# Kernel optimization log

Measured on AMD Instinct MI355X. Metric: run time of the kernel, lower is better.

The kernel has to match this reference:

```python
import jax, jax.numpy as jnp
import numpy as np

N, M1, M2, D, S0, S1 = 60000, 40000, 40000, 64, 10, 20

def setup_inputs() -> dict:
    key = jax.random.key(0)
    ks = jax.random.split(key, 10)
    return {
        "h0": jax.random.normal(ks[0], (N, D), jnp.float32),
        "h1": jax.random.normal(ks[1], (M1, D), jnp.float32),
        "h2": jax.random.normal(ks[2], (M2, D), jnp.float32),
        "nei0": jax.random.randint(ks[3], (N, S0), 0, M1),
        "nei1": jax.random.randint(ks[4], (N, S1), 0, M2),
        "att_w0": jax.random.normal(ks[5], (1, 2 * D), jnp.float32) * 0.15,
        "att_w1": jax.random.normal(ks[6], (1, 2 * D), jnp.float32) * 0.15,
        "fc_w": jax.random.normal(ks[7], (D, D), jnp.float32) * 0.15,
        "fc_b": jnp.zeros((D,), jnp.float32),
        "fus_att_w": jax.random.normal(ks[8], (1, D), jnp.float32) * 0.15,
        "glob_att": jax.random.normal(ks[9], (1, D), jnp.float32) * 0.15,
        "gate": jnp.float32(0.8),
    }

def _nei_att(nei, h, h_refer, att_w):
    # F.embedding gather: [N, S, D]
    nei_emb = h[nei]
    d = h.shape[-1]
    # concat([h_refer, nei_emb]) @ att.T == h_refer@a_ref + nei_emb@a_nei
    a_ref, a_nei = att_w[0, :d], att_w[0, d:]
    scores = (h_refer @ a_ref)[:, None] + nei_emb @ a_nei  # [N, S]
    scores = jax.nn.leaky_relu(scores, 0.01)
    w = jax.nn.softmax(scores, axis=1)  # softmax over neighbors
    return jnp.einsum('ns,nsd->nd', w, nei_emb)

def reference(h0, h1, h2, nei0, nei1, att_w0, att_w1, fc_w, fc_b, fus_att_w, glob_att, gate):
    # intra (per neighbor type) attention + elu
    e0 = jax.nn.elu(_nei_att(nei0, h1, h0, att_w0))
    e1 = jax.nn.elu(_nei_att(nei1, h2, h0, att_w1))
    # fus_att (inter-type semantic attention)
    def beta_of(e):
        sp = jnp.tanh(e @ fc_w.T + fc_b)
        return (sp @ fus_att_w[0]).mean()
    beta = jax.nn.softmax(jnp.stack([beta_of(e0), beta_of(e1)]))
    z_mc = beta[0] * e0 + beta[1] * e1
    # global encoder: softmax over all nodes of all types
    all_nodes = jnp.concatenate([h0, h1, h2], axis=0)
    s = (all_nodes @ glob_att[0]) / jnp.sqrt(jnp.float32(D))
    w = jax.nn.softmax(s, axis=0)[:, None]
    global_embed = (w * all_nodes).sum(axis=0)  # [D]
    # weighted gate fusion
    gv = jax.nn.sigmoid(gate)
    return gv * z_mc + (1.0 - gv) * global_embed
```

## Files before the change

### kernel.cpp

```cpp
#include <hip/hip_runtime.h>
#include <math.h>

#define N_NODES 60000
#define M1_N    40000
#define M2_N    40000
#define DD      64
#define S0_N    10
#define S1_N    20
#define R_TOTAL (N_NODES + M1_N + M2_N)
#define T_H0    (N_NODES / 16)
#define T_H1    (T_H0 + M1_N / 16)
#define T_ALL   (T_H1 + M2_N / 16)
#define PROJ_GRID 2048
#define BETA_GRID 512

typedef __attribute__((ext_vector_type(8))) short short8;
typedef __attribute__((ext_vector_type(4))) float f32x4;

__device__ __forceinline__ float wave_sum(float x) {
#pragma unroll
    for (int o = 32; o >= 1; o >>= 1) x += __shfl_xor(x, o, 64);
    return x;
}
__device__ __forceinline__ float bcast(float v, int l) {
    return __uint_as_float(__builtin_amdgcn_readlane(__float_as_uint(v), l));
}
__device__ __forceinline__ float tanh_fast(float x) {
    return 1.f - 2.f / (__expf(2.f * x) + 1.f);
}
__device__ __forceinline__ unsigned short f2bf(float x) {
    unsigned u = __float_as_uint(x);
    return (unsigned short)((u + 0x7FFFu + ((u >> 16) & 1u)) >> 16);
}
__device__ __forceinline__ float bf2f(unsigned short u) {
    return __uint_as_float(((unsigned)u) << 16);
}

__global__ __launch_bounds__(256) void k_proj(
    const float* __restrict__ h0, const float* __restrict__ h1, const float* __restrict__ h2,
    const float* __restrict__ aw0, const float* __restrict__ aw1, const float* __restrict__ gatt,
    float* __restrict__ part,
    float* __restrict__ p0r0, float* __restrict__ p0r1,
    float* __restrict__ p1, float* __restrict__ p2,
    unsigned short* __restrict__ h1bf, unsigned short* __restrict__ h2bf)
{
    __shared__ float s_wsum[64];
    __shared__ float s_se;
    const int tid = threadIdx.x, lane = tid & 63, wid = tid >> 6;
    if (tid < 64) s_wsum[tid] = 0.f;
    if (tid == 0) s_se = 0.f;
    __syncthreads();

    const int m = lane & 15, quad = lane >> 4;

    short8 b0, b1;
    {
        const float* vsel = 0;
        if (m == 1) vsel = aw0;
        else if (m == 2) vsel = aw1;
        else if (m == 3) vsel = aw0 + DD;
        else if (m == 4) vsel = aw1 + DD;
        else if (m == 0) vsel = gatt;
#pragma unroll
        for (int j = 0; j < 8; j++) {
            b0[j] = vsel ? (short)f2bf(vsel[quad * 8 + j]) : (short)0;
            b1[j] = vsel ? (short)f2bf(vsel[32 + quad * 8 + j]) : (short)0;
        }
    }

    float wacc0[8], wacc1[8];
#pragma unroll
    for (int j = 0; j < 8; j++) { wacc0[j] = 0.f; wacc1[j] = 0.f; }
    float r_se = 0.f;

    const int srcl = (m >> 2) << 4;
    const int rsel = m & 3;

    const int gw = blockIdx.x * 4 + wid, nw = gridDim.x * 4;
    for (int tile = gw; tile < T_ALL; tile += nw) {
        const float* src; int rbase, region;
        if (tile < T_H0)      { src = h0; rbase = tile * 16;          region = 0; }
        else if (tile < T_H1) { src = h1; rbase = (tile - T_H0) * 16; region = 1; }
        else                  { src = h2; rbase = (tile - T_H1) * 16; region = 2; }
        const int row = rbase + m;
        const float4* rpa = (const float4*)(src + (size_t)row * DD + quad * 8);
        const float4* rpb = (const float4*)(src + (size_t)row * DD + 32 + quad * 8);
        const float4 va = rpa[0], vb = rpa[1];
        const float4 vc = rpb[0], vd = rpb[1];

        short8 a0, a1;
        a0[0] = (short)f2bf(va.x); a0[1] = (short)f2bf(va.y);
        a0[2] = (short)f2bf(va.z); a0[3] = (short)f2bf(va.w);
        a0[4] = (short)f2bf(vb.x); a0[5] = (short)f2bf(vb.y);
        a0[6] = (short)f2bf(vb.z); a0[7] = (short)f2bf(vb.w);
        a1[0] = (short)f2bf(vc.x); a1[1] = (short)f2bf(vc.y);
        a1[2] = (short)f2bf(vc.z); a1[3] = (short)f2bf(vc.w);
        a1[4] = (short)f2bf(vd.x); a1[5] = (short)f2bf(vd.y);
        a1[6] = (short)f2bf(vd.z); a1[7] = (short)f2bf(vd.w);

        f32x4 c = {0.f, 0.f, 0.f, 0.f};
        c = __builtin_amdgcn_mfma_f32_16x16x32_bf16(a0, b0, c, 0, 0, 0);
        c = __builtin_amdgcn_mfma_f32_16x16x32_bf16(a1, b1, c, 0, 0, 0);

        const float t0 = __shfl(c[0], srcl, 64);
        const float t1 = __shfl(c[1], srcl, 64);
        const float t2 = __shfl(c[2], srcl, 64);
        const float t3 = __shfl(c[3], srcl, 64);
        const float scr = (rsel == 0) ? t0 : (rsel == 1) ? t1 : (rsel == 2) ? t2 : t3;
        const float es = __expf(scr * 0.125f);
        r_se += es;
        wacc0[0] = fmaf(es, va.x, wacc0[0]); wacc0[1] = fmaf(es, va.y, wacc0[1]);
        wacc0[2] = fmaf(es, va.z, wacc0[2]); wacc0[3] = fmaf(es, va.w, wacc0[3]);
        wacc0[4] = fmaf(es, vb.x, wacc0[4]); wacc0[5] = fmaf(es, vb.y, wacc0[5]);
        wacc0[6] = fmaf(es, vb.z, wacc0[6]); wacc0[7] = fmaf(es, vb.w, wacc0[7]);
        wacc1[0] = fmaf(es, vc.x, wacc1[0]); wacc1[1] = fmaf(es, vc.y, wacc1[1]);
        wacc1[2] = fmaf(es, vc.z, wacc1[2]); wacc1[3] = fmaf(es, vc.w, wacc1[3]);
        wacc1[4] = fmaf(es, vd.x, wacc1[4]); wacc1[5] = fmaf(es, vd.y, wacc1[5]);
        wacc1[6] = fmaf(es, vd.z, wacc1[6]); wacc1[7] = fmaf(es, vd.w, wacc1[7]);

        if (region == 0) {
            if (m == 1) { float4 t = {c[0], c[1], c[2], c[3]}; *(float4*)(p0r0 + rbase + quad * 4) = t; }
            if (m == 2) { float4 t = {c[0], c[1], c[2], c[3]}; *(float4*)(p0r1 + rbase + quad * 4) = t; }
        } else if (region == 1) {
            if (m == 3) { float4 t = {c[0], c[1], c[2], c[3]}; *(float4*)(p1 + rbase + quad * 4) = t; }
            *(short8*)(h1bf + (size_t)row * DD + quad * 8) = a0;
            *(short8*)(h1bf + (size_t)row * DD + 32 + quad * 8) = a1;
        } else {
            if (m == 4) { float4 t = {c[0], c[1], c[2], c[3]}; *(float4*)(p2 + rbase + quad * 4) = t; }
            *(short8*)(h2bf + (size_t)row * DD + quad * 8) = a0;
            *(short8*)(h2bf + (size_t)row * DD + 32 + quad * 8) = a1;
        }
    }

    r_se *= 0.25f;
#pragma unroll
    for (int o = 1; o <= 8; o <<= 1) {
#pragma unroll
        for (int j = 0; j < 8; j++) {
            wacc0[j] += __shfl_xor(wacc0[j], o, 64);
            wacc1[j] += __shfl_xor(wacc1[j], o, 64);
        }
    }
    if (m == 0) {
#pragma unroll
        for (int j = 0; j < 8; j++) {
            atomicAdd(&s_wsum[quad * 8 + j],      wacc0[j]);
            atomicAdd(&s_wsum[32 + quad * 8 + j], wacc1[j]);
        }
    }
    const float se = wave_sum(r_se);
    if (lane == 0) atomicAdd(&s_se, se);
    __syncthreads();
    if (tid < 64) part[tid * PROJ_GRID + blockIdx.x] = s_wsum[tid];
    if (tid == 64) part[64 * PROJ_GRID + blockIdx.x] = s_se;
}

__global__ __launch_bounds__(256) void k_attn(
    const unsigned short* __restrict__ h1bf,
    const int* __restrict__ nei0, const int* __restrict__ nei1,
    const float* __restrict__ p0r0, const float* __restrict__ p0r1,
    const float* __restrict__ p1,
    unsigned short* __restrict__ e0bf, unsigned short* __restrict__ e1bf)
{
    const int tid = threadIdx.x, lane = tid & 63, wid = tid >> 6;
    const int sub = lane & 15, grp = lane >> 4;
    const int gw = blockIdx.x * 4 + wid;
    const int nw = gridDim.x * 4;

    for (int n = gw; n < N_NODES; n += nw) {
        int idx = 0; float w = 0.f;
        if (lane < S0_N) {
            idx = nei0[n * S0_N + lane];
            float sc = p0r0[n] + p1[idx];
            sc = (sc >= 0.f) ? sc : 0.01f * sc;
            w = __expf(sc);
        }
        int r0[3];
#pragma unroll
        for (int j = 0; j < 3; j++) r0[j] = __shfl(idx, 4 * j + grp, 64);
        ushort4 u0[3];
#pragma unroll
        for (int j = 0; j < 3; j++)
            u0[j] = *(const ushort4*)(h1bf + r0[j] * DD + 4 * sub);

        float sv = w;
#pragma unroll
        for (int o = 8; o >= 1; o >>= 1) sv += __shfl_xor(sv, o, 64);
        const float inv = 1.f / bcast(sv, 0);

        float w0[3];
#pragma unroll
        for (int j = 0; j < 3; j++) w0[j] = __shfl(w, 4 * j + grp, 64);

        float4 a = make_float4(0.f, 0.f, 0.f, 0.f);
#pragma unroll
        for (int j = 0; j < 3; j++) {
            a.x = fmaf(w0[j], bf2f(u0[j].x), a.x);
            a.y = fmaf(w0[j], bf2f(u0[j].y), a.y);
            a.z = fmaf(w0[j], bf2f(u0[j].z), a.z);
            a.w = fmaf(w0[j], bf2f(u0[j].w), a.w);
        }
#pragma unroll
        for (int o = 16; o <= 32; o <<= 1) {
            a.x += __shfl_xor(a.x, o, 64); a.y += __shfl_xor(a.y, o, 64);
            a.z += __shfl_xor(a.z, o, 64); a.w += __shfl_xor(a.w, o, 64);
        }
        if (grp == 0) {
            float4 e;
            e.x = a.x * inv; e.y = a.y * inv; e.z = a.z * inv; e.w = a.w * inv;
            e.x = (e.x > 0.f) ? e.x : (__expf(e.x) - 1.f);
            e.y = (e.y > 0.f) ? e.y : (__expf(e.y) - 1.f);
            e.z = (e.z > 0.f) ? e.z : (__expf(e.z) - 1.f);
            e.w = (e.w > 0.f) ? e.w : (__expf(e.w) - 1.f);
            ushort4 s; s.x = f2bf(e.x); s.y = f2bf(e.y); s.z = f2bf(e.z); s.w = f2bf(e.w);
            *(ushort4*)(e0bf + n * DD + 4 * sub) = s;
        }
    }

    for (int n = gw; n < N_NODES; n += nw) {
        int idx = 0; float w = 0.f;
        if (lane < S1_N) {
            idx = nei1[n * S1_N + lane] + M1_N;
            float sc = p0r1[n] + p1[idx];
            sc = (sc >= 0.f) ? sc : 0.01f * sc;
            w = __expf(sc);
        }
        int r1[5];
#pragma unroll
        for (int j = 0; j < 5; j++) r1[j] = __shfl(idx, 4 * j + grp, 64);
        ushort4 u1[5];
#pragma unroll
        for (int j = 0; j < 5; j++)
            u1[j] = *(const ushort4*)(h1bf + r1[j] * DD + 4 * sub);

        float sv = w;
#pragma unroll
        for (int o = 16; o >= 1; o >>= 1) sv += __shfl_xor(sv, o, 64);
        const float inv = 1.f / bcast(sv, 0);

        float w1[5];
#pragma unroll
        for (int j = 0; j < 5; j++) w1[j] = __shfl(w, 4 * j + grp, 64);

        float4 a = make_float4(0.f, 0.f, 0.f, 0.f);
#pragma unroll
        for (int j = 0; j < 5; j++) {
            a.x = fmaf(w1[j], bf2f(u1[j].x), a.x);
            a.y = fmaf(w1[j], bf2f(u1[j].y), a.y);
            a.z = fmaf(w1[j], bf2f(u1[j].z), a.z);
            a.w = fmaf(w1[j], bf2f(u1[j].w), a.w);
        }
#pragma unroll
        for (int o = 16; o <= 32; o <<= 1) {
            a.x += __shfl_xor(a.x, o, 64); a.y += __shfl_xor(a.y, o, 64);
            a.z += __shfl_xor(a.z, o, 64); a.w += __shfl_xor(a.w, o, 64);
        }
        if (grp == 0) {
            float4 e;
            e.x = a.x * inv; e.y = a.y * inv; e.z = a.z * inv; e.w = a.w * inv;
            e.x = (e.x > 0.f) ? e.x : (__expf(e.x) - 1.f);
            e.y = (e.y > 0.f) ? e.y : (__expf(e.y) - 1.f);
            e.z = (e.z > 0.f) ? e.z : (__expf(e.z) - 1.f);
            e.w = (e.w > 0.f) ? e.w : (__expf(e.w) - 1.f);
            ushort4 s; s.x = f2bf(e.x); s.y = f2bf(e.y); s.z = f2bf(e.z); s.w = f2bf(e.w);
            *(ushort4*)(e1bf + n * DD + 4 * sub) = s;
        }
    }
}

__global__ __launch_bounds__(256) void k_beta(
    const unsigned short* __restrict__ e0bf, const unsigned short* __restrict__ e1bf,
    const float* __restrict__ fcw, const float* __restrict__ fcb,
    const float* __restrict__ fus, float* __restrict__ bpart)
{
    __shared__ float s_part[2];
    const int tid = threadIdx.x, lane = tid & 63, wid = tid >> 6;
    if (tid < 2) s_part[tid] = 0.f;
    const int m = lane & 15, q = lane >> 4;

    short8 bfr[4][2];
    float fb[4], fu[4];
#pragma unroll
    for (int t = 0; t < 4; t++) {
        const float* wrow = fcw + (t * 16 + m) * DD;
#pragma unroll
        for (int h = 0; h < 2; h++) {
            const float* p = wrow + h * 32 + q * 8;
#pragma unroll
            for (int j = 0; j < 8; j++) bfr[t][h][j] = (short)f2bf(p[j]);
        }
        fb[t] = fcb[t * 16 + m];
        fu[t] = fus[t * 16 + m];
    }
    __syncthreads();

    float rb0 = 0.f, rb1 = 0.f;
    const int gw = blockIdx.x * 4 + wid;
    const int nw = gridDim.x * 4;
    for (int tile = gw; tile < N_NODES / 16; tile += nw) {
        const int rowbase = (tile * 16 + m) * DD + q * 8;
        {
            const short8 a0 = *(const short8*)(e0bf + rowbase);
            const short8 a1 = *(const short8*)(e0bf + rowbase + 32);
            f32x4 c[4];
#pragma unroll
            for (int t = 0; t < 4; t++) {
                c[t] = f32x4{0.f, 0.f, 0.f, 0.f};
                c[t] = __builtin_amdgcn_mfma_f32_16x16x32_bf16(a0, bfr[t][0], c[t], 0, 0, 0);
                c[t] = __builtin_amdgcn_mfma_f32_16x16x32_bf16(a1, bfr[t][1], c[t], 0, 0, 0);
            }
#pragma unroll
            for (int t = 0; t < 4; t++)
#pragma unroll
                for (int j = 0; j < 4; j++)
                    rb0 += tanh_fast(c[t][j] + fb[t]) * fu[t];
        }
        {
            const short8 a0 = *(const short8*)(e1bf + rowbase);
            const short8 a1 = *(const short8*)(e1bf + rowbase + 32);
            f32x4 c[4];
#pragma unroll
            for (int t = 0; t < 4; t++) {
                c[t] = f32x4{0.f, 0.f, 0.f, 0.f};
                c[t] = __builtin_amdgcn_mfma_f32_16x16x32_bf16(a0, bfr[t][0], c[t], 0, 0, 0);
                c[t] = __builtin_amdgcn_mfma_f32_16x16x32_bf16(a1, bfr[t][1], c[t], 0, 0, 0);
            }
#pragma unroll
            for (int t = 0; t < 4; t++)
#pragma unroll
                for (int j = 0; j < 4; j++)
                    rb1 += tanh_fast(c[t][j] + fb[t]) * fu[t];
        }
    }
    const float b0 = wave_sum(rb0);
    const float b1 = wave_sum(rb1);
    if (lane == 0) { atomicAdd(&s_part[0], b0); atomicAdd(&s_part[1], b1); }
    __syncthreads();
    if (tid == 0) {
        bpart[blockIdx.x]             = s_part[0];
        bpart[BETA_GRID + blockIdx.x] = s_part[1];
    }
}

__global__ __launch_bounds__(256) void k_reduce(
    const float* __restrict__ part, const float* __restrict__ bpart,
    float* __restrict__ accum)
{
    const int tid = threadIdx.x, lane = tid & 63, wid = tid >> 6;
    if (wid == 0) {
        float t0 = 0.f, t1 = 0.f;
#pragma unroll
        for (int k = 0; k < BETA_GRID / 64; k++) {
            t0 += bpart[lane + 64 * k];
            t1 += bpart[BETA_GRID + lane + 64 * k];
        }
        t0 = wave_sum(t0); t1 = wave_sum(t1);
        if (lane == 0) { accum[0] = t0; accum[1] = t1; }
    }
    for (int j = wid; j < 65; j += 4) {
        float s = 0.f;
#pragma unroll
        for (int k = 0; k < PROJ_GRID / 64; k++)
            s += part[j * PROJ_GRID + lane + 64 * k];
        s = wave_sum(s);
        if (lane == 0) {
            if (j < 64) accum[4 + j] = s;
            else        accum[2] = s;
        }
    }
}

__global__ __launch_bounds__(256) void k_out(
    const unsigned short* __restrict__ e0bf, const unsigned short* __restrict__ e1bf,
    const float* __restrict__ accum, const float* __restrict__ gate,
    float* __restrict__ out)
{
    const int i = blockIdx.x * 256 + threadIdx.x;
    const float b0 = accum[0] * (1.f / N_NODES);
    const float b1 = accum[1] * (1.f / N_NODES);
    const float mx = fmaxf(b0, b1);
    const float eb0 = __expf(b0 - mx), eb1 = __expf(b1 - mx);
    const float gv  = 1.f / (1.f + __expf(-gate[0]));
    const float c0  = gv * eb0 / (eb0 + eb1);
    const float c1  = gv * eb1 / (eb0 + eb1);
    const float cg  = (1.f - gv) / accum[2];

    const float4 av = ((const float4*)(accum + 4))[i & 15];
    const ushort4 ua = ((const ushort4*)e0bf)[i];
    const ushort4 ub = ((const ushort4*)e1bf)[i];
    float4 o;
    o.x = c0 * bf2f(ua.x) + c1 * bf2f(ub.x) + cg * av.x;
    o.y = c0 * bf2f(ua.y) + c1 * bf2f(ub.y) + cg * av.y;
    o.z = c0 * bf2f(ua.z) + c1 * bf2f(ub.z) + cg * av.z;
    o.w = c0 * bf2f(ua.w) + c1 * bf2f(ub.w) + cg * av.w;
    ((float4*)out)[i] = o;
}

extern "C" void kernel_launch(void* const* d_in, const int* in_sizes, int n_in,
                              void* d_out, int out_size, void* d_ws, size_t ws_size,
                              hipStream_t stream) {
    (void)in_sizes; (void)n_in; (void)out_size; (void)ws_size;
    const float* h0   = (const float*)d_in[0];
    const float* h1   = (const float*)d_in[1];
    const float* h2   = (const float*)d_in[2];
    const int*   nei0 = (const int*)  d_in[3];
    const int*   nei1 = (const int*)  d_in[4];
    const float* aw0  = (const float*)d_in[5];
    const float* aw1  = (const float*)d_in[6];
    const float* fcw  = (const float*)d_in[7];
    const float* fcb  = (const float*)d_in[8];
    const float* fus  = (const float*)d_in[9];
    const float* gatt = (const float*)d_in[10];
    const float* gate = (const float*)d_in[11];
    float* out = (float*)d_out;

    float* ws    = (float*)d_ws;
    float* accum = ws;
    float* p0r0  = ws + 256;
    float* p0r1  = p0r0 + N_NODES;
    float* p1    = p0r1 + N_NODES;
    float* p2    = p1 + M1_N;
    unsigned short* h1bf = (unsigned short*)(p2 + M2_N);
    unsigned short* h2bf = h1bf + (size_t)M1_N * DD;
    unsigned short* e0bf = h2bf + (size_t)M2_N * DD;
    unsigned short* e1bf = e0bf + (size_t)N_NODES * DD;
    float* part  = (float*)(e1bf + (size_t)N_NODES * DD);
    float* bpart = part + 65 * PROJ_GRID;

    k_proj<<<PROJ_GRID, 256, 0, stream>>>(h0, h1, h2, aw0, aw1, gatt, part,
                                          p0r0, p0r1, p1, p2, h1bf, h2bf);
    k_attn<<<2048, 256, 0, stream>>>(h1bf, nei0, nei1, p0r0, p0r1, p1, e0bf, e1bf);
    k_beta<<<BETA_GRID, 256, 0, stream>>>(e0bf, e1bf, fcw, fcb, fus, bpart);
    k_reduce<<<1, 256, 0, stream>>>(part, bpart, accum);
    k_out<<<(N_NODES * DD / 4) / 256, 256, 0, stream>>>(e0bf, e1bf, accum, gate, out);
}
```

Before: 182.3 us.

## Process two nodes per wavefront in neighbor attention, with nontemporal index loads and stores

Each wavefront in k_attn now handles two destination nodes at once, one per 32-lane half, instead of one node per wave. This fills lanes that sat idle when S0=10 or S1=20 and raises gather parallelism per wave, with the neighbor weights accumulated into two separate accumulators. Neighbor index loads and the bf16 output stores use nontemporal hints so they bypass cache retention. The cost is more registers per thread (up to 10 gathered rows plus two accumulators) and extra select and shuffle logic.

```diff
diff --git a/kernel.cpp b/kernel.cpp
--- a/kernel.cpp
+++ b/kernel.cpp
@@ -34,6 +34,9 @@
 }
 __device__ __forceinline__ float bf2f(unsigned short u) {
     return __uint_as_float(((unsigned)u) << 16);
+}
+__device__ __forceinline__ float elu(float x) {
+    return (x > 0.f) ? x : (__expf(x) - 1.f);
 }
 
 __global__ __launch_bounds__(256) void k_proj(
@@ -164,106 +167,141 @@
 {
     const int tid = threadIdx.x, lane = tid & 63, wid = tid >> 6;
     const int sub = lane & 15, grp = lane >> 4;
+    const int h = lane >> 5, hl = lane & 31;
     const int gw = blockIdx.x * 4 + wid;
     const int nw = gridDim.x * 4;
 
-    for (int n = gw; n < N_NODES; n += nw) {
+    for (int n0 = gw * 2; n0 < N_NODES; n0 += nw * 2) {
+        const int n = n0 + h;
         int idx = 0; float w = 0.f;
-        if (lane < S0_N) {
-            idx = nei0[n * S0_N + lane];
+        if (hl < S0_N) {
+            idx = __builtin_nontemporal_load(nei0 + n * S0_N + hl);
             float sc = p0r0[n] + p1[idx];
             sc = (sc >= 0.f) ? sc : 0.01f * sc;
             w = __expf(sc);
         }
-        int r0[3];
-#pragma unroll
-        for (int j = 0; j < 3; j++) r0[j] = __shfl(idx, 4 * j + grp, 64);
-        ushort4 u0[3];
-#pragma unroll
-        for (int j = 0; j < 3; j++)
-            u0[j] = *(const ushort4*)(h1bf + r0[j] * DD + 4 * sub);
+        int rows[5], srcs[5];
+#pragma unroll
+        for (int j = 0; j < 5; j++) {
+            const int s = 4 * j + grp;
+            srcs[j] = (s < S0_N) ? s : (32 - S0_N + s);
+            rows[j] = __shfl(idx, srcs[j], 64);
+        }
+        ushort4 u[5];
+#pragma unroll
+        for (int j = 0; j < 5; j++)
+            u[j] = *(const ushort4*)(h1bf + rows[j] * DD + 4 * sub);
 
         float sv = w;
 #pragma unroll
         for (int o = 8; o >= 1; o >>= 1) sv += __shfl_xor(sv, o, 64);
-        const float inv = 1.f / bcast(sv, 0);
-
-        float w0[3];
-#pragma unroll
-        for (int j = 0; j < 3; j++) w0[j] = __shfl(w, 4 * j + grp, 64);
-
-        float4 a = make_float4(0.f, 0.f, 0.f, 0.f);
-#pragma unroll
-        for (int j = 0; j < 3; j++) {
-            a.x = fmaf(w0[j], bf2f(u0[j].x), a.x);
-            a.y = fmaf(w0[j], bf2f(u0[j].y), a.y);
-            a.z = fmaf(w0[j], bf2f(u0[j].z), a.z);
-            a.w = fmaf(w0[j], bf2f(u0[j].w), a.w);
+        const float invA = 1.f / bcast(sv, 0);
+        const float invB = 1.f / bcast(sv, 32);
+
+        float4 aA = make_float4(0.f, 0.f, 0.f, 0.f);
+        float4 aB = make_float4(0.f, 0.f, 0.f, 0.f);
+#pragma unroll
+        for (int j = 0; j < 5; j++) {
+            const float ws = __uint_as_float(
+                (unsigned)__shfl(__float_as_int(w), srcs[j], 64));
+            const bool isA = (4 * j + grp) < S0_N;
+            float4 x;
+            x.x = bf2f(u[j].x); x.y = bf2f(u[j].y);
+            x.z = bf2f(u[j].z); x.w = bf2f(u[j].w);
+            if (isA) {
+                aA.x = fmaf(ws, x.x, aA.x); aA.y = fmaf(ws, x.y, aA.y);
+                aA.z = fmaf(ws, x.z, aA.z); aA.w = fmaf(ws, x.w, aA.w);
+            } else {
+                aB.x = fmaf(ws, x.x, aB.x); aB.y = fmaf(ws, x.y, aB.y);
+                aB.z = fmaf(ws, x.z, aB.z); aB.w = fmaf(ws, x.w, aB.w);
+            }
         }
 #pragma unroll
         for (int o = 16; o <= 32; o <<= 1) {
-            a.x += __shfl_xor(a.x, o, 64); a.y += __shfl_xor(a.y, o, 64);
-            a.z += __shfl_xor(a.z, o, 64); a.w += __shfl_xor(a.w, o, 64);
+            aA.x += __shfl_xor(aA.x, o, 64); aA.y += __shfl_xor(aA.y, o, 64);
+            aA.z += __shfl_xor(aA.z, o, 64); aA.w += __shfl_xor(aA.w, o, 64);
+            aB.x += __shfl_xor(aB.x, o, 64); aB.y += __shfl_xor(aB.y, o, 64);
+            aB.z += __shfl_xor(aB.z, o, 64); aB.w += __shfl_xor(aB.w, o, 64);
         }
         if (grp == 0) {
-            float4 e;
-            e.x = a.x * inv; e.y = a.y * inv; e.z = a.z * inv; e.w = a.w * inv;
-            e.x = (e.x > 0.f) ? e.x : (__expf(e.x) - 1.f);
-            e.y = (e.y > 0.f) ? e.y : (__expf(e.y) - 1.f);
-            e.z = (e.z > 0.f) ? e.z : (__expf(e.z) - 1.f);
-            e.w = (e.w > 0.f) ? e.w : (__expf(e.w) - 1.f);
-            ushort4 s; s.x = f2bf(e.x); s.y = f2bf(e.y); s.z = f2bf(e.z); s.w = f2bf(e.w);
-            *(ushort4*)(e0bf + n * DD + 4 * sub) = s;
-        }
-    }
-
-    for (int n = gw; n < N_NODES; n += nw) {
+            ushort4 s;
+            s.x = f2bf(elu(aA.x * invA)); s.y = f2bf(elu(aA.y * invA));
+            s.z = f2bf(elu(aA.z * invA)); s.w = f2bf(elu(aA.w * invA));
+            __builtin_nontemporal_store(*(unsigned long long*)&s,
+                (unsigned long long*)(e0bf + n0 * DD + 4 * sub));
+        } else if (grp == 1) {
+            ushort4 s;
+            s.x = f2bf(elu(aB.x * invB)); s.y = f2bf(elu(aB.y * invB));
+            s.z = f2bf(elu(aB.z * invB)); s.w = f2bf(elu(aB.w * invB));
+            __builtin_nontemporal_store(*(unsigned long long*)&s,
+                (unsigned long long*)(e0bf + (n0 + 1) * DD + 4 * sub));
+        }
+    }
+
+    for (int n0 = gw * 2; n0 < N_NODES; n0 += nw * 2) {
+        const int n = n0 + h;
         int idx = 0; float w = 0.f;
-        if (lane < S1_N) {
-            idx = nei1[n * S1_N + lane] + M1_N;
+        if (hl < S1_N) {
+            idx = __builtin_nontemporal_load(nei1 + n * S1_N + hl) + M1_N;
             float sc = p0r1[n] + p1[idx];
             sc = (sc >= 0.f) ? sc : 0.01f * sc;
             w = __expf(sc);
         }
-        int r1[5];
-#pragma unroll
-        for (int j = 0; j < 5; j++) r1[j] = __shfl(idx, 4 * j + grp, 64);
-        ushort4 u1[5];
-#pragma unroll
-        for (int j = 0; j < 5; j++)
-            u1[j] = *(const ushort4*)(h1bf + r1[j] * DD + 4 * sub);
+        int rows[10], srcs[10];
+#pragma unroll
+        for (int j = 0; j < 10; j++) {
+            const int s = 4 * j + grp;
+            srcs[j] = (s < S1_N) ? s : (32 - S1_N + s);
+            rows[j] = __shfl(idx, srcs[j], 64);
+        }
+        ushort4 u[10];
+#pragma unroll
+        for (int j = 0; j < 10; j++)
+            u[j] = *(const ushort4*)(h1bf + rows[j] * DD + 4 * sub);
 
         float sv = w;
 #pragma unroll
         for (int o = 16; o >= 1; o >>= 1) sv += __shfl_xor(sv, o, 64);
-        const float inv = 1.f / bcast(sv, 0);
-
-        float w1[5];
-#pragma unroll
-        for (int j = 0; j < 5; j++) w1[j] = __shfl(w, 4 * j + grp, 64);
-
-        float4 a = make_float4(0.f, 0.f, 0.f, 0.f);
-#pragma unroll
-        for (int j = 0; j < 5; j++) {
-            a.x = fmaf(w1[j], bf2f(u1[j].x), a.x);
-            a.y = fmaf(w1[j], bf2f(u1[j].y), a.y);
-            a.z = fmaf(w1[j], bf2f(u1[j].z), a.z);
-            a.w = fmaf(w1[j], bf2f(u1[j].w), a.w);
+        const float invA = 1.f / bcast(sv, 0);
+        const float invB = 1.f / bcast(sv, 32);
+
+        float4 aA = make_float4(0.f, 0.f, 0.f, 0.f);
+        float4 aB = make_float4(0.f, 0.f, 0.f, 0.f);
+#pragma unroll
+        for (int j = 0; j < 10; j++) {
+            const float ws = __uint_as_float(
+                (unsigned)__shfl(__float_as_int(w), srcs[j], 64));
+            const bool isA = (4 * j + grp) < S1_N;
+            float4 x;
+            x.x = bf2f(u[j].x); x.y = bf2f(u[j].y);
+            x.z = bf2f(u[j].z); x.w = bf2f(u[j].w);
+            if (isA) {
+                aA.x = fmaf(ws, x.x, aA.x); aA.y = fmaf(ws, x.y, aA.y);
+                aA.z = fmaf(ws, x.z, aA.z); aA.w = fmaf(ws, x.w, aA.w);
+            } else {
+                aB.x = fmaf(ws, x.x, aB.x); aB.y = fmaf(ws, x.y, aB.y);
+                aB.z = fmaf(ws, x.z, aB.z); aB.w = fmaf(ws, x.w, aB.w);
+            }
         }
 #pragma unroll
         for (int o = 16; o <= 32; o <<= 1) {
-            a.x += __shfl_xor(a.x, o, 64); a.y += __shfl_xor(a.y, o, 64);
-            a.z += __shfl_xor(a.z, o, 64); a.w += __shfl_xor(a.w, o, 64);
+            aA.x += __shfl_xor(aA.x, o, 64); aA.y += __shfl_xor(aA.y, o, 64);
+            aA.z += __shfl_xor(aA.z, o, 64); aA.w += __shfl_xor(aA.w, o, 64);
+            aB.x += __shfl_xor(aB.x, o, 64); aB.y += __shfl_xor(aB.y, o, 64);
+            aB.z += __shfl_xor(aB.z, o, 64); aB.w += __shfl_xor(aB.w, o, 64);
         }
         if (grp == 0) {
-            float4 e;
-            e.x = a.x * inv; e.y = a.y * inv; e.z = a.z * inv; e.w = a.w * inv;
-            e.x = (e.x > 0.f) ? e.x : (__expf(e.x) - 1.f);
-            e.y = (e.y > 0.f) ? e.y : (__expf(e.y) - 1.f);
-            e.z = (e.z > 0.f) ? e.z : (__expf(e.z) - 1.f);
-            e.w = (e.w > 0.f) ? e.w : (__expf(e.w) - 1.f);
-            ushort4 s; s.x = f2bf(e.x); s.y = f2bf(e.y); s.z = f2bf(e.z); s.w = f2bf(e.w);
-            *(ushort4*)(e1bf + n * DD + 4 * sub) = s;
+            ushort4 s;
+            s.x = f2bf(elu(aA.x * invA)); s.y = f2bf(elu(aA.y * invA));
+            s.z = f2bf(elu(aA.z * invA)); s.w = f2bf(elu(aA.w * invA));
+            __builtin_nontemporal_store(*(unsigned long long*)&s,
+                (unsigned long long*)(e1bf + n0 * DD + 4 * sub));
+        } else if (grp == 1) {
+            ushort4 s;
+            s.x = f2bf(elu(aB.x * invB)); s.y = f2bf(elu(aB.y * invB));
+            s.z = f2bf(elu(aB.z * invB)); s.w = f2bf(elu(aB.w * invB));
+            __builtin_nontemporal_store(*(unsigned long long*)&s,
+                (unsigned long long*)(e1bf + (n0 + 1) * DD + 4 * sub));
         }
     }
 }
@@ -284,10 +322,10 @@
     for (int t = 0; t < 4; t++) {
         const float* wrow = fcw + (t * 16 + m) * DD;
 #pragma unroll
-        for (int h = 0; h < 2; h++) {
-            const float* p = wrow + h * 32 + q * 8;
-#pragma unroll
-            for (int j = 0; j < 8; j++) bfr[t][h][j] = (short)f2bf(p[j]);
+        for (int hh = 0; hh < 2; hh++) {
+            const float* p = wrow + hh * 32 + q * 8;
+#pragma unroll
+            for (int j = 0; j < 8; j++) bfr[t][hh][j] = (short)f2bf(p[j]);
         }
         fb[t] = fcb[t * 16 + m];
         fu[t] = fus[t * 16 + m];
```

Measured after the change: 182.5 us. About the same (+0.1%).
